# Performance work log

Hardware: AMD Instinct MI355X
Metric: run time of the kernel (lower is better)

## Reference

```python
import jax, jax.numpy as jnp
import numpy as np

DIM = 1024
HEADS = 16
HEAD_DIM = DIM // HEADS
SCALE = HEAD_DIM ** -0.5


def apply_rope(x, theta=10000.0):
    # x: [b, h, n, d]
    n, d = x.shape[2], x.shape[3]
    seq = jnp.arange(n, dtype=jnp.float32)
    inv = 1.0 / (theta ** (jnp.arange(0, d, 2, dtype=jnp.float32) / d))  # [d/2]
    freqs = seq[:, None] * inv[None, :]  # [n, d/2]
    cos = jnp.cos(freqs)[None, None]  # [1,1,n,d/2]
    sin = jnp.sin(freqs)[None, None]
    x1, x2 = jnp.split(x, 2, axis=-1)
    return jnp.concatenate([x1 * cos - x2 * sin, x1 * sin + x2 * cos], axis=-1)


def setup_inputs() -> dict:
    key = jax.random.key(0)
    ks = jax.random.split(key, 7)
    s = DIM ** -0.5
    return {
        "x": jax.random.normal(ks[0], (2, 2048, DIM), dtype=jnp.float32),
        "Wqkv": jax.random.normal(ks[1], (3 * DIM, DIM), dtype=jnp.float32) * s,
        "bqkv": jax.random.normal(ks[2], (3 * DIM,), dtype=jnp.float32) * 0.02,
        "Wpre": jax.random.normal(ks[3], (HEADS, HEADS), dtype=jnp.float32) * HEADS ** -0.5,
        "Wpost": jax.random.normal(ks[4], (HEADS, HEADS), dtype=jnp.float32) * HEADS ** -0.5,
        "Wout": jax.random.normal(ks[5], (DIM, DIM), dtype=jnp.float32) * s,
        "bout": jax.random.normal(ks[6], (DIM,), dtype=jnp.float32) * 0.02,
    }


def reference(x, Wqkv, bqkv, Wpre, Wpost, Wout, bout):
    b, n, _ = x.shape
    qkv = x @ Wqkv.T + bqkv  # [b, n, 3*dim]
    q, k, v = jnp.split(qkv, 3, axis=-1)
    # [b, n, dim] -> [b, h, n, d]
    reshape = lambda t: t.reshape(b, n, HEADS, HEAD_DIM).transpose(0, 2, 1, 3)
    q, k, v = reshape(q), reshape(k), reshape(v)
    q = apply_rope(q)
    k = apply_rope(k)
    logits = jnp.einsum('bhid,bhjd->bhij', q, k) * SCALE
    # pre-softmax talking heads: Linear(heads->heads), y[...,g] = sum_h x[...,h] * Wpre[g,h]
    logits = jnp.einsum('bhij,gh->bgij', logits, Wpre)
    attn = jax.nn.softmax(logits, axis=-1)
    attn = jnp.einsum('bhij,gh->bgij', attn, Wpost)
    out = jnp.einsum('bhij,bhjd->bhid', attn, v)
    out = out.transpose(0, 2, 1, 3).reshape(b, n, DIM)
    return out @ Wout.T + bout
```

## Files before the change

### kernel.cpp

```cpp
#include <hip/hip_runtime.h>
#include <cstddef>
#include <cstdint>

#define SEQ    2048
#define DMODEL 1024
#define NHEAD  16
#define HDIM   64
#define SCALE  0.125f
#define LOG2E  1.4426950408889634f

typedef _Float16 f16;
typedef unsigned short u16;
typedef unsigned int   u32;
typedef __attribute__((ext_vector_type(8))) _Float16 h8v;
typedef __attribute__((ext_vector_type(4))) _Float16 h4v;
typedef __attribute__((ext_vector_type(4))) float    f4v;

__device__ __forceinline__ u32 pkh(float a, float b) {
    u16 x = __builtin_bit_cast(u16, (f16)a);
    u16 y = __builtin_bit_cast(u16, (f16)b);
    return (u32)x | ((u32)y << 16);
}

__device__ __forceinline__ float fexp2(float x) {
#if __has_builtin(__builtin_amdgcn_exp2f)
    return __builtin_amdgcn_exp2f(x);
#else
    return exp2f(x);
#endif
}

__device__ __forceinline__ f4v mfma32(h8v a, h8v b, f4v c) {
    return __builtin_amdgcn_mfma_f32_16x16x32_f16(a, b, c, 0, 0, 0);
}
__device__ __forceinline__ f4v mfma16(h4v a, h4v b, f4v c) {
    return __builtin_amdgcn_mfma_f32_16x16x16f16(a, b, c, 0, 0, 0);
}

__global__ __launch_bounds__(256)
void cvt_f16_kernel(const float* __restrict__ x, const float* __restrict__ Wqkv,
                    const float* __restrict__ Wout,
                    f16* __restrict__ Xh, f16* __restrict__ Wqh, f16* __restrict__ Woh)
{
    size_t i = ((size_t)blockIdx.x * 256 + threadIdx.x) * 8;
    const float* src; f16* dst; size_t off;
    if (i < 4194304)      { src = x;    dst = Xh;  off = i; }
    else if (i < 7340032) { src = Wqkv; dst = Wqh; off = i - 4194304; }
    else                  { src = Wout; dst = Woh; off = i - 7340032; }
    float4 a = *(const float4*)&src[off];
    float4 b = *(const float4*)&src[off + 4];
    uint4 o;
    o.x = pkh(a.x, a.y); o.y = pkh(a.z, a.w);
    o.z = pkh(b.x, b.y); o.w = pkh(b.z, b.w);
    *(uint4*)&dst[off] = o;
}

__global__ __launch_bounds__(256)
void gemm_f16_kernel(const f16* __restrict__ A, const f16* __restrict__ B,
                     const float* __restrict__ bias, void* __restrict__ Cout,
                     int N, int K, int mode)
{
    __shared__ __align__(16) char Asb[8192];
    __shared__ __align__(16) char Bsb[8192];
    int tid = threadIdx.x;
    int w = tid >> 6, l = tid & 63, lr = l & 15, lc = l >> 4;
    int row0 = blockIdx.y * 128, col0 = blockIdx.x * 128;
    int wr = (w >> 1) * 64, wc = (w & 1) * 64;

    f4v acc[4][4];
    #pragma unroll
    for (int m = 0; m < 4; ++m)
        #pragma unroll
        for (int n = 0; n < 4; ++n) acc[m][n] = (f4v){0.f, 0.f, 0.f, 0.f};

    int r0 = tid >> 2, k0s = tid & 3;
    int r1 = (tid + 256) >> 2, k1s = tid & 3;

    uint4 ra0, ra1, rb0, rb1;
    ra0 = *(const uint4*)&A[(size_t)(row0 + r0) * K + k0s * 8];
    ra1 = *(const uint4*)&A[(size_t)(row0 + r1) * K + k1s * 8];
    rb0 = *(const uint4*)&B[(size_t)(col0 + r0) * K + k0s * 8];
    rb1 = *(const uint4*)&B[(size_t)(col0 + r1) * K + k1s * 8];

    int NT = K >> 5;
    for (int kt = 0; kt < NT; ++kt) {
        *(uint4*)(Asb + r0 * 64 + ((k0s ^ (r0 & 3)) << 4)) = ra0;
        *(uint4*)(Asb + r1 * 64 + ((k1s ^ (r1 & 3)) << 4)) = ra1;
        *(uint4*)(Bsb + r0 * 64 + ((k0s ^ (r0 & 3)) << 4)) = rb0;
        *(uint4*)(Bsb + r1 * 64 + ((k1s ^ (r1 & 3)) << 4)) = rb1;
        if (kt + 1 < NT) {
            int kk = (kt + 1) * 32;
            ra0 = *(const uint4*)&A[(size_t)(row0 + r0) * K + kk + k0s * 8];
            ra1 = *(const uint4*)&A[(size_t)(row0 + r1) * K + kk + k1s * 8];
            rb0 = *(const uint4*)&B[(size_t)(col0 + r0) * K + kk + k0s * 8];
            rb1 = *(const uint4*)&B[(size_t)(col0 + r1) * K + kk + k1s * 8];
        }
        __syncthreads();
        h8v af[4], bf[4];
        #pragma unroll
        for (int m = 0; m < 4; ++m) {
            int row = wr + m * 16 + lr;
            af[m] = *(h8v*)(Asb + row * 64 + ((lc ^ (row & 3)) << 4));
        }
        #pragma unroll
        for (int n = 0; n < 4; ++n) {
            int col = wc + n * 16 + lr;
            bf[n] = *(h8v*)(Bsb + col * 64 + ((lc ^ (col & 3)) << 4));
        }
        #pragma unroll
        for (int m = 0; m < 4; ++m)
            #pragma unroll
            for (int n = 0; n < 4; ++n)
                acc[m][n] = mfma32(af[m], bf[n], acc[m][n]);
        __syncthreads();
    }

    #pragma unroll
    for (int m = 0; m < 4; ++m)
        #pragma unroll
        for (int r = 0; r < 4; ++r) {
            int row = row0 + wr + m * 16 + lc * 4 + r;
            #pragma unroll
            for (int n = 0; n < 4; ++n) {
                int col = col0 + wc + n * 16 + lr;
                float v = acc[m][n][r] + bias[col];
                if (mode == 0) ((f16*)Cout)[(size_t)row * N + col] = (f16)v;
                else           ((float*)Cout)[(size_t)row * N + col] = v;
            }
        }
}

__global__ __launch_bounds__(256)
void pack_qk_kernel(const f16* __restrict__ QKVh, f16* __restrict__ Qh, f16* __restrict__ Kh)
{
    int gid = blockIdx.x * 256 + threadIdx.x;
    int i     = gid & 15;
    int t8    = (gid >> 4) & 3;
    int h     = (gid >> 6) & 15;
    int rh    = (gid >> 10) & 255;
    int which = (gid >> 18) & 1;
    int row = rh * 16 + i;
    int pos = row & (SEQ - 1);
    int b   = row >> 11;
    f16* dst = which ? Kh : Qh;

    h8v x1 = *(const h8v*)&QKVh[(size_t)row * 3072 + which * 1024 + h * 64 + t8 * 8];
    h8v x2 = *(const h8v*)&QKVh[(size_t)row * 3072 + which * 1024 + h * 64 + t8 * 8 + 32];

    float y1[8], y2[8];
    #pragma unroll
    for (int e = 0; e < 8; ++e) {
        int t = t8 * 8 + e;
        float inv = exp2f((float)(-2 * t) * (0.015625f * 13.287712379549449f));
        float ang = (float)pos * inv;
        float c, s;
        sincosf(ang, &s, &c);
        float a1 = (float)x1[e], a2 = (float)x2[e];
        y1[e] = a1 * c - a2 * s;
        y2[e] = a1 * s + a2 * c;
    }
    int it = pos >> 4;
    size_t b0 = (((((size_t)(b*128 + it)*16 + h)*2 + 0)*4 + t8)*16 + i)*8;
    size_t b1 = (((((size_t)(b*128 + it)*16 + h)*2 + 1)*4 + t8)*16 + i)*8;
    uint4 o0, o1;
    o0.x = pkh(y1[0], y1[1]); o0.y = pkh(y1[2], y1[3]);
    o0.z = pkh(y1[4], y1[5]); o0.w = pkh(y1[6], y1[7]);
    o1.x = pkh(y2[0], y2[1]); o1.y = pkh(y2[2], y2[3]);
    o1.z = pkh(y2[4], y2[5]); o1.w = pkh(y2[6], y2[7]);
    *(uint4*)(dst + b0) = o0;
    *(uint4*)(dst + b1) = o1;
}

__global__ __launch_bounds__(256)
void pack_v_kernel(const f16* __restrict__ QKVh, f16* __restrict__ Vt)
{
    int gid = blockIdx.x * 256 + threadIdx.x;
    int dd = gid & 15;
    int jc = (gid >> 4) & 3;
    int dt = (gid >> 6) & 3;
    int g  = (gid >> 8) & 15;
    int jt = (gid >> 12) & 63;
    int b  = (gid >> 18) & 1;
    int d = g * 64 + dt * 16 + dd;
    f16 v[8];
    #pragma unroll
    for (int e = 0; e < 8; ++e) {
        int j = jt * 32 + jc * 8 + e;
        v[e] = QKVh[(size_t)(b * SEQ + j) * 3072 + 2048 + d];
    }
    size_t off = ((((((size_t)b*64 + jt)*16 + g)*4 + dt)*4 + jc)*16 + dd)*8;
    uint4 o;
    o.x = pkh((float)v[0], (float)v[1]); o.y = pkh((float)v[2], (float)v[3]);
    o.z = pkh((float)v[4], (float)v[5]); o.w = pkh((float)v[6], (float)v[7]);
    *(uint4*)(Vt + off) = o;
}

__global__ __launch_bounds__(256)
void pack_ctx_kernel(const f16* __restrict__ Cp, f16* __restrict__ Ch)
{
    size_t i = ((size_t)blockIdx.x * 256 + threadIdx.x) * 8;
    h8v p0 = *(const h8v*)&Cp[i];
    h8v p1 = *(const h8v*)&Cp[i + 4194304];
    h8v p2 = *(const h8v*)&Cp[i + 8388608];
    h8v p3 = *(const h8v*)&Cp[i + 12582912];
    float s[8];
    #pragma unroll
    for (int e = 0; e < 8; ++e)
        s[e] = (float)p0[e] + (float)p1[e] + (float)p2[e] + (float)p3[e];
    uint4 o;
    o.x = pkh(s[0], s[1]); o.y = pkh(s[2], s[3]);
    o.z = pkh(s[4], s[5]); o.w = pkh(s[6], s[7]);
    *(uint4*)&Ch[i] = o;
}

template<int FULL>
__global__ __launch_bounds__(1024, FULL ? 1 : 2)
void attn_core(const f16* __restrict__ Qh, const f16* __restrict__ Kh,
               const f16* __restrict__ Vt, const float* __restrict__ Wpre,
               const float* __restrict__ Wpost, const float* __restrict__ Zp,
               float* __restrict__ Zout, f16* __restrict__ Octx)
{
    __shared__ __align__(16) char ss[65536];
    __shared__ __align__(16) char es[FULL ? 65536 : 16];

    int tid = threadIdx.x;
    int wv = tid >> 6;
    int l  = tid & 63;
    int lr = l & 15;
    int lc = l >> 4;

    int bid   = blockIdx.x;
    int it2   = bid & 63;
    int b     = (bid >> 6) & 1;
    int split = bid >> 7;

    h4v wpre4;
    #pragma unroll
    for (int e = 0; e < 4; ++e) wpre4[e] = (f16)(Wpre[lr * 16 + lc * 4 + e] * (SCALE * LOG2E));
    h4v wpost;
    if (FULL) {
        #pragma unroll
        for (int e = 0; e < 4; ++e) wpost[e] = (f16)Wpost[lr * 16 + lc * 4 + e];
    }

    h8v qf[2][2];
    #pragma unroll
    for (int itl = 0; itl < 2; ++itl)
        #pragma unroll
        for (int ks = 0; ks < 2; ++ks) {
            size_t off = ((((size_t)((b*128 + it2*2 + itl)*16 + wv)*2 + ks)*4 + lc)*16 + lr)*8;
            qf[itl][ks] = *(const h8v*)(Qh + off);
        }

    float m4[2][4];
    if (FULL) {
        float* zrd = (float*)ss;
        if (tid < 512) {
            int itl = tid >> 8, g = (tid >> 4) & 15, i = tid & 15;
            size_t idx = (size_t)(b * 16 + g) * SEQ + it2 * 32 + itl * 16 + i;
            zrd[tid] = log2f(Zp[idx] + Zp[65536 + idx] + Zp[131072 + idx] + Zp[196608 + idx]);
        }
        __syncthreads();
        #pragma unroll
        for (int itl = 0; itl < 2; ++itl)
            #pragma unroll
            for (int r = 0; r < 4; ++r)
                m4[itl][r] = zrd[itl * 256 + (lc * 4 + r) * 16 + lr];
        __syncthreads();
    }

    f4v pv[2][4];
    if (FULL) {
        #pragma unroll
        for (int itl = 0; itl < 2; ++itl)
            #pragma unroll
            for (int dt = 0; dt < 4; ++dt) pv[itl][dt] = (f4v){0.f, 0.f, 0.f, 0.f};
    }
    float zacc[2][4] = {};

    int j0beg = split * 512;
    int jtbeg = j0beg >> 4;
    int jvbeg = j0beg >> 5;

    for (int s = 0; s < 8; ++s) {
        h8v vf0[4];
        if (FULL) {
            int jt32 = jvbeg + s * 2;
            #pragma unroll
            for (int dt = 0; dt < 4; ++dt) {
                size_t voff = (((((size_t)(b*64 + jt32)*16 + wv)*4 + dt)*4 + lc)*16 + lr)*8;
                vf0[dt] = *(const h8v*)(Vt + voff);
            }
        }
        #pragma unroll
        for (int jsp = 0; jsp < 2; ++jsp) {
            h8v kf[2][2];
            #pragma unroll
            for (int js2 = 0; js2 < 2; ++js2)
                #pragma unroll
                for (int ks = 0; ks < 2; ++ks) {
                    int jt = jtbeg + s * 4 + jsp * 2 + js2;
                    size_t off = ((((size_t)((b*128 + jt)*16 + wv)*2 + ks)*4 + lc)*16 + lr)*8;
                    kf[js2][ks] = *(const h8v*)(Kh + off);
                }
            #pragma unroll
            for (int itl = 0; itl < 2; ++itl)
                #pragma unroll
                for (int js2 = 0; js2 < 2; ++js2) {
                    f4v q = (f4v){0.f, 0.f, 0.f, 0.f};
                    q = mfma32(qf[itl][0], kf[js2][0], q);
                    q = mfma32(qf[itl][1], kf[js2][1], q);
                    int js = jsp * 2 + js2;
                    #pragma unroll
                    for (int r = 0; r < 4; ++r) {
                        int i = lc * 4 + r;
                        int addr = itl * 32768 + ((wv >> 2) * 4 + js) * 2048
                                 + i * 128 + ((lr ^ i) << 3) + (wv & 3) * 2;
                        *(u16*)(ss + addr) = __builtin_bit_cast(u16, (f16)q[r]);
                    }
                }
        }
        __syncthreads();

        #pragma unroll
        for (int itl = 0; itl < 2; ++itl) {
            u32 a2p[4][2];
            #pragma unroll
            for (int tt = 0; tt < 4; ++tt) {
                int t = wv * 4 + tt;
                int addr = itl * 32768 + (lc * 4 + (t >> 4)) * 2048
                         + lr * 128 + (((t & 15) ^ lr) << 3);
                union { uint2 u; h4v v; } cv;
                cv.u = *(uint2*)(ss + addr);
                f4v s1 = mfma16(wpre4, cv.v, (f4v){0.f, 0.f, 0.f, 0.f});
                if (!FULL) {
                    #pragma unroll
                    for (int r = 0; r < 4; ++r) zacc[itl][r] += fexp2(s1[r]);
                } else {
                    h4v pf;
                    #pragma unroll
                    for (int r = 0; r < 4; ++r) pf[r] = (f16)fexp2(s1[r] - m4[itl][r]);
                    f4v a2 = mfma16(wpost, pf, (f4v){0.f, 0.f, 0.f, 0.f});
                    #pragma unroll
                    for (int r = 0; r < 4; ++r) {
                        u32 v = (u32)__builtin_bit_cast(u16, (f16)a2[r]);
                        if (tt & 1) a2p[r][tt >> 1] |= v << 16;
                        else        a2p[r][tt >> 1]  = v;
                    }
                }
            }
            if (FULL) {
                #pragma unroll
                for (int r = 0; r < 4; ++r) {
                    int gq = lc * 4 + r;
                    int off = itl * 32768 + gq * 2048 + lr * 128
                            + ((wv * 8) ^ ((lr & 7) << 4));
                    *(uint2*)(es + off) = make_uint2(a2p[r][0], a2p[r][1]);
                }
            }
        }
        h8v vf1[4];
        if (FULL) {
            int jt32 = jvbeg + s * 2 + 1;
            #pragma unroll
            for (int dt = 0; dt < 4; ++dt) {
                size_t voff = (((((size_t)(b*64 + jt32)*16 + wv)*4 + dt)*4 + lc)*16 + lr)*8;
                vf1[dt] = *(const h8v*)(Vt + voff);
            }
        }
        __syncthreads();

        if (FULL) {
            #pragma unroll
            for (int itl = 0; itl < 2; ++itl) {
                h8v af0 = *(h8v*)(es + itl * 32768 + wv * 2048 + lr * 128
                                  + ((0 * 64 + lc * 16) ^ ((lr & 7) << 4)));
                h8v af1 = *(h8v*)(es + itl * 32768 + wv * 2048 + lr * 128
                                  + ((1 * 64 + lc * 16) ^ ((lr & 7) << 4)));
                #pragma unroll
                for (int dt = 0; dt < 4; ++dt)
                    pv[itl][dt] = mfma32(af0, vf0[dt], pv[itl][dt]);
                #pragma unroll
                for (int dt = 0; dt < 4; ++dt)
                    pv[itl][dt] = mfma32(af1, vf1[dt], pv[itl][dt]);
            }
        }
    }

    if (!FULL) {
        float* zrd = (float*)ss;
        #pragma unroll
        for (int itl = 0; itl < 2; ++itl)
            #pragma unroll
            for (int r = 0; r < 4; ++r)
                zrd[itl * 4096 + ((lc * 4 + r) * 16 + lr) * 16 + wv] = zacc[itl][r];
        __syncthreads();
        if (tid < 512) {
            int itl = tid >> 8, gi = tid & 255;
            float z = 0.f;
            #pragma unroll
            for (int w2 = 0; w2 < 16; ++w2) z += zrd[itl * 4096 + gi * 16 + w2];
            int g = gi >> 4, i = gi & 15;
            Zout[(size_t)split * 65536 + (size_t)(b * 16 + g) * SEQ + it2 * 32 + itl * 16 + i] = z;
        }
    } else {
        f16* dst = Octx + (size_t)split * 4194304;
        #pragma unroll
        for (int itl = 0; itl < 2; ++itl)
            #pragma unroll
            for (int dt = 0; dt < 4; ++dt)
                #pragma unroll
                for (int r = 0; r < 4; ++r) {
                    int row = it2 * 32 + itl * 16 + lc * 4 + r;
                    int col = wv * 64 + dt * 16 + lr;
                    dst[(size_t)(b * SEQ + row) * DMODEL + col] = (f16)pv[itl][dt][r];
                }
    }
}

extern "C" void kernel_launch(void* const* d_in, const int* in_sizes, int n_in,
                              void* d_out, int out_size, void* d_ws, size_t ws_size,
                              hipStream_t stream)
{
    const float* x     = (const float*)d_in[0];
    const float* Wqkv  = (const float*)d_in[1];
    const float* bqkv  = (const float*)d_in[2];
    const float* Wpre  = (const float*)d_in[3];
    const float* Wpost = (const float*)d_in[4];
    const float* Wout  = (const float*)d_in[5];
    const float* bout  = (const float*)d_in[6];
    float* out = (float*)d_out;

    float* ws = (float*)d_ws;
    f16*   QKVh = (f16*)(ws);
    f16*   CTXp = (f16*)(ws);
    f16*   Xh   = (f16*)(ws + 8388608);
    f16*   Wqh  = (f16*)(ws + 10485760);
    f16*   Woh  = (f16*)(ws + 12058624);
    f16*   Qh   = (f16*)(ws + 12582912);
    f16*   Kh   = (f16*)(ws + 14680064);
    f16*   Vt   = (f16*)(ws + 16777216);
    f16*   Ch   = (f16*)(ws + 18874368);
    float* Zp   = ws + 19922944;

    dim3 blk(256);
    cvt_f16_kernel<<<4096, blk, 0, stream>>>(x, Wqkv, Wout, Xh, Wqh, Woh);
    gemm_f16_kernel<<<dim3(24, 32), blk, 0, stream>>>(Xh, Wqh, bqkv, (void*)QKVh, 3072, 1024, 0);
    pack_qk_kernel<<<2048, blk, 0, stream>>>(QKVh, Qh, Kh);
    pack_v_kernel<<<2048, blk, 0, stream>>>(QKVh, Vt);
    attn_core<0><<<512, dim3(1024), 0, stream>>>(Qh, Kh, Vt, Wpre, Wpost, nullptr, Zp, nullptr);
    attn_core<1><<<512, dim3(1024), 0, stream>>>(Qh, Kh, Vt, Wpre, Wpost, Zp, nullptr, CTXp);
    pack_ctx_kernel<<<2048, blk, 0, stream>>>(CTXp, Ch);
    gemm_f16_kernel<<<dim3(8, 32), blk, 0, stream>>>(Ch, Woh, bout, (void*)out, 1024, 1024, 1);
}
```

Baseline: 209.9 us.

## Halve key splits in full attention pass, precompute RoPE table, fold max into MFMA

The second attention pass now covers 1024 keys per block over 16 steps with 256 blocks instead of 4 splits of 512, so the context partial-sum reduction only adds two partials. RoPE cos/sin values are precomputed once into a table by a small kernel, replacing per-element sincos in pack_qk. The negative log-normalizer is folded into the MFMA accumulator init, removing a subtraction per element. Fewer blocks (256 on a large GPU) lowers parallelism and occupancy for the full pass, and the extra kernel launch adds overhead.

```diff
diff --git a/kernel.cpp b/kernel.cpp
--- a/kernel.cpp
+++ b/kernel.cpp
@@ -35,6 +35,17 @@
 }
 __device__ __forceinline__ f4v mfma16(h4v a, h4v b, f4v c) {
     return __builtin_amdgcn_mfma_f32_16x16x16f16(a, b, c, 0, 0, 0);
+}
+
+__global__ __launch_bounds__(256)
+void rope_tab_kernel(float2* __restrict__ tab)
+{
+    int gid = blockIdx.x * 256 + threadIdx.x;
+    int pos = gid >> 5, t = gid & 31;
+    float inv = exp2f((float)(-2 * t) * (0.015625f * 13.287712379549449f));
+    float c, s;
+    sincosf((float)pos * inv, &s, &c);
+    tab[gid] = make_float2(c, s);
 }
 
 __global__ __launch_bounds__(256)
@@ -131,7 +142,8 @@
 }
 
 __global__ __launch_bounds__(256)
-void pack_qk_kernel(const f16* __restrict__ QKVh, f16* __restrict__ Qh, f16* __restrict__ Kh)
+void pack_qk_kernel(const f16* __restrict__ QKVh, const float2* __restrict__ tab,
+                    f16* __restrict__ Qh, f16* __restrict__ Kh)
 {
     int gid = blockIdx.x * 256 + threadIdx.x;
     int i     = gid & 15;
@@ -151,13 +163,10 @@
     #pragma unroll
     for (int e = 0; e < 8; ++e) {
         int t = t8 * 8 + e;
-        float inv = exp2f((float)(-2 * t) * (0.015625f * 13.287712379549449f));
-        float ang = (float)pos * inv;
-        float c, s;
-        sincosf(ang, &s, &c);
+        float2 cs = tab[pos * 32 + t];
         float a1 = (float)x1[e], a2 = (float)x2[e];
-        y1[e] = a1 * c - a2 * s;
-        y2[e] = a1 * s + a2 * c;
+        y1[e] = a1 * cs.x - a2 * cs.y;
+        y2[e] = a1 * cs.y + a2 * cs.x;
     }
     int it = pos >> 4;
     size_t b0 = (((((size_t)(b*128 + it)*16 + h)*2 + 0)*4 + t8)*16 + i)*8;
@@ -201,12 +210,10 @@
     size_t i = ((size_t)blockIdx.x * 256 + threadIdx.x) * 8;
     h8v p0 = *(const h8v*)&Cp[i];
     h8v p1 = *(const h8v*)&Cp[i + 4194304];
-    h8v p2 = *(const h8v*)&Cp[i + 8388608];
-    h8v p3 = *(const h8v*)&Cp[i + 12582912];
     float s[8];
     #pragma unroll
     for (int e = 0; e < 8; ++e)
-        s[e] = (float)p0[e] + (float)p1[e] + (float)p2[e] + (float)p3[e];
+        s[e] = (float)p0[e] + (float)p1[e];
     uint4 o;
     o.x = pkh(s[0], s[1]); o.y = pkh(s[2], s[3]);
     o.z = pkh(s[4], s[5]); o.w = pkh(s[6], s[7]);
@@ -252,7 +259,7 @@
             qf[itl][ks] = *(const h8v*)(Qh + off);
         }
 
-    float m4[2][4];
+    f4v m4n[2];
     if (FULL) {
         float* zrd = (float*)ss;
         if (tid < 512) {
@@ -265,7 +272,7 @@
         for (int itl = 0; itl < 2; ++itl)
             #pragma unroll
             for (int r = 0; r < 4; ++r)
-                m4[itl][r] = zrd[itl * 256 + (lc * 4 + r) * 16 + lr];
+                m4n[itl][r] = -zrd[itl * 256 + (lc * 4 + r) * 16 + lr];
         __syncthreads();
     }
 
@@ -278,11 +285,12 @@
     }
     float zacc[2][4] = {};
 
-    int j0beg = split * 512;
+    const int NSTEP = FULL ? 16 : 8;
+    int j0beg = split * (FULL ? 1024 : 512);
     int jtbeg = j0beg >> 4;
     int jvbeg = j0beg >> 5;
 
-    for (int s = 0; s < 8; ++s) {
+    for (int s = 0; s < NSTEP; ++s) {
         h8v vf0[4];
         if (FULL) {
             int jt32 = jvbeg + s * 2;
@@ -332,14 +340,15 @@
                          + lr * 128 + (((t & 15) ^ lr) << 3);
                 union { uint2 u; h4v v; } cv;
                 cv.u = *(uint2*)(ss + addr);
-                f4v s1 = mfma16(wpre4, cv.v, (f4v){0.f, 0.f, 0.f, 0.f});
                 if (!FULL) {
+                    f4v s1 = mfma16(wpre4, cv.v, (f4v){0.f, 0.f, 0.f, 0.f});
                     #pragma unroll
                     for (int r = 0; r < 4; ++r) zacc[itl][r] += fexp2(s1[r]);
                 } else {
+                    f4v s1 = mfma16(wpre4, cv.v, m4n[itl]);
                     h4v pf;
                     #pragma unroll
-                    for (int r = 0; r < 4; ++r) pf[r] = (f16)fexp2(s1[r] - m4[itl][r]);
+                    for (int r = 0; r < 4; ++r) pf[r] = (f16)fexp2(s1[r]);
                     f4v a2 = mfma16(wpost, pf, (f4v){0.f, 0.f, 0.f, 0.f});
                     #pragma unroll
                     for (int r = 0; r < 4; ++r) {
@@ -442,14 +451,16 @@
     f16*   Vt   = (f16*)(ws + 16777216);
     f16*   Ch   = (f16*)(ws + 18874368);
     float* Zp   = ws + 19922944;
+    float2* Tab = (float2*)(ws + 20185088);
 
     dim3 blk(256);
+    rope_tab_kernel<<<256, blk, 0, stream>>>(Tab);
     cvt_f16_kernel<<<4096, blk, 0, stream>>>(x, Wqkv, Wout, Xh, Wqh, Woh);
     gemm_f16_kernel<<<dim3(24, 32), blk, 0, stream>>>(Xh, Wqh, bqkv, (void*)QKVh, 3072, 1024, 0);
-    pack_qk_kernel<<<2048, blk, 0, stream>>>(QKVh, Qh, Kh);
+    pack_qk_kernel<<<2048, blk, 0, stream>>>(QKVh, Tab, Qh, Kh);
     pack_v_kernel<<<2048, blk, 0, stream>>>(QKVh, Vt);
     attn_core<0><<<512, dim3(1024), 0, stream>>>(Qh, Kh, Vt, Wpre, Wpost, nullptr, Zp, nullptr);
-    attn_core<1><<<512, dim3(1024), 0, stream>>>(Qh, Kh, Vt, Wpre, Wpost, Zp, nullptr, CTXp);
+    attn_core<1><<<256, dim3(1024), 0, stream>>>(Qh, Kh, Vt, Wpre, Wpost, Zp, nullptr, CTXp);
     pack_ctx_kernel<<<2048, blk, 0, stream>>>(CTXp, Ch);
     gemm_f16_kernel<<<dim3(8, 32), blk, 0, stream>>>(Ch, Woh, bout, (void*)out, 1024, 1024, 1);
 }
```

Result: no change. 209.5 us (-0.2%).
